# Performance work log

Measured on AMD Instinct MI355X. Metric: run time of the kernel, lower is better.

## Reference

```python
import jax, jax.numpy as jnp
import numpy as np


def setup_inputs() -> dict:
    key = jax.random.key(0)
    ks = jax.random.split(key, 12)
    L, B, T, E, H = 8, 256, 8, 1024, 1024
    w_scale = 1.0 / np.sqrt(E + H)  # keep gates out of saturation (mimics Linear init scale)
    inp = {
        "x": jax.random.normal(ks[0], (B, T, E), dtype=jnp.float32),
        "h0": jax.random.normal(ks[1], (L, B, H), dtype=jnp.float32),
        "c0": jax.random.normal(ks[2], (L, B, H), dtype=jnp.float32),
        "Wu": jax.random.normal(ks[3], (L, E + H, H), dtype=jnp.float32) * w_scale,
        "bu": jax.random.normal(ks[4], (L, H), dtype=jnp.float32) * w_scale,
        "Wf": jax.random.normal(ks[5], (L, E + H, H), dtype=jnp.float32) * w_scale,
        "bf": jax.random.normal(ks[6], (L, H), dtype=jnp.float32) * w_scale,
        "Wo": jax.random.normal(ks[7], (L, E + H, H), dtype=jnp.float32) * w_scale,
        "bo": jax.random.normal(ks[8], (L, H), dtype=jnp.float32) * w_scale,
        "Wc": jax.random.normal(ks[9], (L, E + H, H), dtype=jnp.float32) * w_scale,
        "bc": jax.random.normal(ks[10], (L, H), dtype=jnp.float32) * w_scale,
    }
    return inp


def reference(x, h0, c0, Wu, bu, Wf, bf, Wo, bo, Wc, bc):
    # x: [B,T,E]; h0,c0: [L,B,H]; W*: [L,E+H,H]; b*: [L,H]
    # Faithful to source: num_cells layers, time loop over first num_cells steps (T == L here).
    L = h0.shape[0]
    h = jnp.transpose(h0, (1, 0, 2))  # [B,L,H]
    c = jnp.transpose(c0, (1, 0, 2))

    def step(carry, xt):  # xt: [B,E]
        h, c = carry
        inp = xt
        hs, cs = [], []
        for l in range(L):
            zh = jnp.concatenate([inp, h[:, l]], axis=-1)  # [B, E+H]
            u = jax.nn.sigmoid(zh @ Wu[l] + bu[l])
            f = jax.nn.sigmoid(zh @ Wf[l] + bf[l])
            o = jax.nn.sigmoid(zh @ Wo[l] + bo[l])
            c_tilde = jnp.tanh(zh @ Wc[l] + bc[l])
            c_new = f * c[:, l] + u * c_tilde
            h_new = o * jnp.tanh(c_new)
            hs.append(h_new)
            cs.append(c_new)
            inp = h_new
        h = jnp.stack(hs, axis=1)
        c = jnp.stack(cs, axis=1)
        return (h, c), (h_new, c_new)  # emit top-layer h_t, c_t

    (_, _), (hs, cs) = jax.lax.scan(step, (h, c), jnp.transpose(x, (1, 0, 2)))
    hidden_states = jnp.transpose(hs, (1, 0, 2))  # [B,T,H]
    memory_states = jnp.transpose(cs, (1, 0, 2))
    h_t = hidden_states[:, -1:, :]  # [B,1,H], matches torch slice-shape
    c_t = memory_states[:, -1:, :]
    return hidden_states, memory_states, h_t, c_t
```

## Files before the change

### kernel.cpp

```cpp
#include <hip/hip_runtime.h>
#include <hip/hip_bf16.h>

#define B_ 256
#define T_ 8
#define E_ 1024
#define H_ 1024
#define L_ 8
#define KD 2048
#define ND 4096

#define BM 256
#define BN 128
#define BK 64
#define ABYTES 32768
#define BUFBYTES 49152
#define NT (KD / BK)

typedef __bf16 bf16x8 __attribute__((ext_vector_type(8)));
typedef float floatx4 __attribute__((ext_vector_type(4)));

__device__ __forceinline__ float sigm(float x) { return 1.f / (1.f + __expf(-x)); }
__device__ __forceinline__ float tanh_(float x) { return 1.f - 2.f / (__expf(2.f * x) + 1.f); }

__device__ __forceinline__ void async16(const void* g, void* l) {
    __builtin_amdgcn_global_load_lds(
        (const __attribute__((address_space(1))) void*)g,
        (__attribute__((address_space(3))) void*)l, 16, 0, 0);
}

__global__ __launch_bounds__(256) void prep_weights_g(
    const float* __restrict__ src, __hip_bfloat16* __restrict__ WTt, int g)
{
    __shared__ float sm[64][33];
    int bid = blockIdx.x;
    int jt = bid & 31;
    int kt = (bid >> 5) & 31;
    int l  = bid >> 10;
    int tid = threadIdx.x;
    int j4  = tid & 7;
    int kl0 = tid >> 3;
#pragma unroll
    for (int r = 0; r < 2; ++r) {
        int kl = kl0 + r * 32;
        float4 v = *(const float4*)&src[((size_t)(l * KD + kt * 64 + kl)) * 1024 + jt * 32 + j4 * 4];
        sm[kl][j4 * 4 + 0] = v.x;
        sm[kl][j4 * 4 + 1] = v.y;
        sm[kl][j4 * 4 + 2] = v.z;
        sm[kl][j4 * 4 + 3] = v.w;
    }
    __syncthreads();
    int jw = tid >> 3;
    int ch = tid & 7;
    int kc = ch * 8;
    bf16x8 v;
#pragma unroll
    for (int i = 0; i < 8; ++i)
        v[i] = (__bf16)sm[kc + i][jw];
    int n   = jt * 32 + jw;
    int nn  = n * 4 + g;
    int nb  = nn >> 7;
    int row = nn & 127;
    int cs  = ch ^ (row & 7);
    size_t off = ((((size_t)l * 32 + nb) * 32 + kt) * 128 + row) * 64 + (size_t)cs * 8;
    *(bf16x8*)&WTt[off] = v;
}

__global__ __launch_bounds__(256) void prep_misc(
    const float* __restrict__ x,  const float* __restrict__ h0,
    const float* __restrict__ c0,
    const float* __restrict__ bu, const float* __restrict__ bfv,
    const float* __restrict__ bo, const float* __restrict__ bc,
    __hip_bfloat16* __restrict__ xbf, __hip_bfloat16* __restrict__ hb0,
    float* __restrict__ cbuf, float* __restrict__ bcat)
{
    size_t i = (size_t)blockIdx.x * 256 + threadIdx.x;
    const size_t NX = (size_t)B_ * T_ * E_;
    const size_t NH = (size_t)L_ * B_ * H_;
    if (i < NX) {
        xbf[i] = __float2bfloat16(x[i]);
    } else if (i < NX + NH) {
        size_t j = i - NX; hb0[j] = __float2bfloat16(h0[j]);
    } else if (i < NX + 2 * NH) {
        size_t j = i - NX - NH; cbuf[j] = c0[j];
    } else if (i < NX + 2 * NH + (size_t)L_ * ND) {
        size_t j = i - NX - 2 * NH;
        int l = (int)(j >> 12); int n = (int)(j & 4095);
        int jj = n >> 2; int g = n & 3;
        const float* bs = (g == 0) ? bu : (g == 1) ? bfv : (g == 2) ? bo : bc;
        bcat[j] = bs[l * 1024 + jj];
    }
}

__global__ __launch_bounds__(512) void lstm_step(
    int d, int tmin,
    const __hip_bfloat16* __restrict__ xbf,
    const __hip_bfloat16* __restrict__ WTt,
    const float* __restrict__ bcat,
    __hip_bfloat16* __restrict__ hb0,
    __hip_bfloat16* __restrict__ hb1,
    float* __restrict__ cbuf,
    float* __restrict__ out)
{
    __shared__ __align__(16) char smraw[3][BUFBYTES];

    int cell = blockIdx.x >> 5;
    int nb   = blockIdx.x & 31;
    int t = tmin + cell;
    int l = d - t;

    const __hip_bfloat16* hread  = (t & 1) ? hb1 : hb0;
    __hip_bfloat16*       hwrite = (t & 1) ? hb0 : hb1;

    const __hip_bfloat16* A1; int sA1;
    if (l == 0) { A1 = xbf + (size_t)t * E_;               sA1 = T_ * E_; }
    else        { A1 = hwrite + (size_t)(l - 1) * B_ * H_; sA1 = H_; }
    const __hip_bfloat16* A2 = hread + (size_t)l * B_ * H_;
    const __hip_bfloat16* Bt = WTt + (((size_t)l * 32 + nb) * 32) * 128 * 64;

    int tid  = threadIdx.x;
    int lane = tid & 63;
    int wid  = tid >> 6;
    int wm = (wid & 3) * 64;
    int wn = (wid >> 2) * 64;
    int lr   = lane & 15;
    int quad = lane >> 4;

    int srow = tid >> 3;
    int c    = (tid & 7) ^ (srow & 7);
    const __hip_bfloat16* pA1[4];
    const __hip_bfloat16* pA2[4];
#pragma unroll
    for (int s = 0; s < 4; ++s) {
        int row = s * 64 + srow;
        pA1[s] = A1 + (size_t)row * sA1 + c * 8;
        pA2[s] = A2 + (size_t)row * H_ + c * 8 - E_;
    }
    const __hip_bfloat16* pB0 = Bt + (size_t)tid * 8;
    int ldsWaveOff = wid * 1024;

    auto stage = [&](int kt, int buf) {
        char* dst = smraw[buf];
        int k0 = kt * BK;
        bool first = (k0 < E_);
#pragma unroll
        for (int s = 0; s < 4; ++s) {
            const __hip_bfloat16* g = (first ? pA1[s] : pA2[s]) + k0;
            async16(g, dst + s * 8192 + ldsWaveOff);
        }
#pragma unroll
        for (int s = 0; s < 2; ++s) {
            async16(pB0 + (size_t)kt * 8192 + s * 4096, dst + ABYTES + s * 8192 + ldsWaveOff);
        }
    };

    floatx4 acc[4][4];
    floatx4 zero = {0.f, 0.f, 0.f, 0.f};
#pragma unroll
    for (int mi = 0; mi < 4; ++mi)
#pragma unroll
        for (int ni = 0; ni < 4; ++ni) acc[mi][ni] = zero;

    stage(0, 0);
    stage(1, 1);
    asm volatile("s_waitcnt vmcnt(6)" ::: "memory");
    __builtin_amdgcn_s_barrier();

    for (int kt = 0; kt < NT; ++kt) {
        const int cur = kt % 3;
        const __hip_bfloat16* sm  = (const __hip_bfloat16*)smraw[cur];
        const __hip_bfloat16* smB = sm + ABYTES / 2;

        {
            int xo = ((quad ^ (lr & 7)) * 8);
            bf16x8 af[4], bfr[4];
#pragma unroll
            for (int mi = 0; mi < 4; ++mi)
                af[mi] = *(const bf16x8*)&sm[(wm + mi * 16 + lr) * 64 + xo];
#pragma unroll
            for (int ni = 0; ni < 4; ++ni)
                bfr[ni] = *(const bf16x8*)&smB[(wn + ni * 16 + lr) * 64 + xo];
            if (kt + 2 < NT) stage(kt + 2, (kt + 2) % 3);
            __builtin_amdgcn_s_barrier();
            asm volatile("s_waitcnt lgkmcnt(0)" ::: "memory");
            __builtin_amdgcn_s_setprio(1);
#pragma unroll
            for (int mi = 0; mi < 4; ++mi)
#pragma unroll
                for (int ni = 0; ni < 4; ++ni)
                    acc[mi][ni] = __builtin_amdgcn_mfma_f32_16x16x32_bf16(
                        af[mi], bfr[ni], acc[mi][ni], 0, 0, 0);
            __builtin_amdgcn_s_setprio(0);
            __builtin_amdgcn_s_barrier();
        }

        {
            int xo = (((4 + quad) ^ (lr & 7)) * 8);
            bf16x8 af[4], bfr[4];
#pragma unroll
            for (int mi = 0; mi < 4; ++mi)
                af[mi] = *(const bf16x8*)&sm[(wm + mi * 16 + lr) * 64 + xo];
#pragma unroll
            for (int ni = 0; ni < 4; ++ni)
                bfr[ni] = *(const bf16x8*)&smB[(wn + ni * 16 + lr) * 64 + xo];
            __builtin_amdgcn_s_barrier();
            asm volatile("s_waitcnt lgkmcnt(0)" ::: "memory");
            __builtin_amdgcn_s_setprio(1);
#pragma unroll
            for (int mi = 0; mi < 4; ++mi)
#pragma unroll
                for (int ni = 0; ni < 4; ++ni)
                    acc[mi][ni] = __builtin_amdgcn_mfma_f32_16x16x32_bf16(
                        af[mi], bfr[ni], acc[mi][ni], 0, 0, 0);
            __builtin_amdgcn_s_setprio(0);
            if (kt < NT - 1) {
                if (kt + 2 < NT) { asm volatile("s_waitcnt vmcnt(6)" ::: "memory"); }
                else             { asm volatile("s_waitcnt vmcnt(0)" ::: "memory"); }
            }
            __builtin_amdgcn_s_barrier();
        }
    }

    float* outH  = out;
    float* outC  = out + (size_t)B_ * T_ * H_;
    float* outHt = out + 2 * (size_t)B_ * T_ * H_;
    float* outCt = outHt + (size_t)B_ * H_;
    auto sC = (float(*)[BN + 4])smraw[0];

    for (int q = 0; q < 4; ++q) {
        __syncthreads();
        if ((wid & 3) == q) {
#pragma unroll
            for (int mi = 0; mi < 4; ++mi)
#pragma unroll
                for (int ni = 0; ni < 4; ++ni)
#pragma unroll
                    for (int r = 0; r < 4; ++r)
                        sC[mi * 16 + quad * 4 + r][wn + ni * 16 + lr] = acc[mi][ni][r];
        }
        __syncthreads();
#pragma unroll
        for (int s = 0; s < 4; ++s) {
            int p = tid + s * 512;
            int r  = p >> 5;
            int jj = p & 31;
            float4 v  = *(float4*)&sC[r][jj * 4];
            float4 bb = *(const float4*)&bcat[(size_t)l * ND + nb * BN + jj * 4];
            float u  = sigm(v.x + bb.x);
            float f  = sigm(v.y + bb.y);
            float o  = sigm(v.z + bb.z);
            float ct = tanh_(v.w + bb.w);
            int b = q * 64 + r;
            int j = nb * 32 + jj;
            size_t ci = ((size_t)l * B_ + b) * H_ + j;
            float cn = f * cbuf[ci] + u * ct;
            cbuf[ci] = cn;
            float hn = o * tanh_(cn);
            hwrite[ci] = __float2bfloat16(hn);
            if (l == L_ - 1) {
                size_t oi = ((size_t)b * T_ + t) * H_ + j;
                outH[oi] = hn;
                outC[oi] = cn;
                if (t == T_ - 1) {
                    outHt[(size_t)b * H_ + j] = hn;
                    outCt[(size_t)b * H_ + j] = cn;
                }
            }
        }
    }
}

extern "C" void kernel_launch(void* const* d_in, const int* in_sizes, int n_in,
                              void* d_out, int out_size, void* d_ws, size_t ws_size,
                              hipStream_t stream)
{
    const float* x   = (const float*)d_in[0];
    const float* h0  = (const float*)d_in[1];
    const float* c0  = (const float*)d_in[2];
    const float* Wu  = (const float*)d_in[3];
    const float* bu  = (const float*)d_in[4];
    const float* Wf  = (const float*)d_in[5];
    const float* bfv = (const float*)d_in[6];
    const float* Wo  = (const float*)d_in[7];
    const float* bo  = (const float*)d_in[8];
    const float* Wc  = (const float*)d_in[9];
    const float* bc  = (const float*)d_in[10];
    float* out = (float*)d_out;

    char* ws = (char*)d_ws;
    __hip_bfloat16* WTt  = (__hip_bfloat16*)(ws);
    float*          bcat = (float*)(ws + 134217728);
    __hip_bfloat16* xbf  = (__hip_bfloat16*)(ws + 134348800);
    __hip_bfloat16* hb0  = (__hip_bfloat16*)(ws + 138543104);
    __hip_bfloat16* hb1  = (__hip_bfloat16*)(ws + 142737408);
    float*          cbuf = (float*)(ws + 146931712);

    hipLaunchKernelGGL(prep_weights_g, dim3(8192), dim3(256), 0, stream, Wu, WTt, 0);
    hipLaunchKernelGGL(prep_weights_g, dim3(8192), dim3(256), 0, stream, Wf, WTt, 1);
    hipLaunchKernelGGL(prep_weights_g, dim3(8192), dim3(256), 0, stream, Wo, WTt, 2);
    hipLaunchKernelGGL(prep_weights_g, dim3(8192), dim3(256), 0, stream, Wc, WTt, 3);
    size_t n2 = (size_t)2097152 * 3 + (size_t)L_ * ND;
    hipLaunchKernelGGL(prep_misc, dim3((unsigned)((n2 + 255) / 256)), dim3(256), 0, stream,
                       x, h0, c0, bu, bfv, bo, bc, xbf, hb0, cbuf, bcat);

    for (int dg = 0; dg <= (T_ - 1) + (L_ - 1); ++dg) {
        int tmin = dg > L_ - 1 ? dg - (L_ - 1) : 0;
        int tmax = dg < T_ - 1 ? dg : T_ - 1;
        int nc = tmax - tmin + 1;
        hipLaunchKernelGGL(lstm_step, dim3(nc * 32), dim3(512), 0, stream,
                           dg, tmin, xbf, WTt, bcat, hb0, hb1, cbuf, out);
    }
}
```

Baseline: 954.9 us.

## Split batch into two M-tiles with 256-thread blocks and double buffering

Halves the M tile from 256 to 128 rows so each wavefront diagonal launches twice as many blocks (64 per cell) with 256 threads each, raising CU occupancy on the small diagonals. The LDS pipeline drops from triple to double buffering, with the prefetch moved after both k-substeps behind a single barrier. Halving the tile also halves per-block reuse of the weight tiles, so weight traffic from L2/HBM doubles, and the pipeline now has less prefetch depth.

```diff
diff --git a/kernel.cpp b/kernel.cpp
--- a/kernel.cpp
+++ b/kernel.cpp
@@ -9,11 +9,11 @@
 #define KD 2048
 #define ND 4096
 
-#define BM 256
+#define BM 128
 #define BN 128
 #define BK 64
-#define ABYTES 32768
-#define BUFBYTES 49152
+#define ABYTES 16384
+#define BUFBYTES 32768
 #define NT (KD / BK)
 
 typedef __bf16 bf16x8 __attribute__((ext_vector_type(8)));
@@ -91,7 +91,7 @@
     }
 }
 
-__global__ __launch_bounds__(512) void lstm_step(
+__global__ __launch_bounds__(256) void lstm_step(
     int d, int tmin,
     const __hip_bfloat16* __restrict__ xbf,
     const __hip_bfloat16* __restrict__ WTt,
@@ -101,10 +101,11 @@
     float* __restrict__ cbuf,
     float* __restrict__ out)
 {
-    __shared__ __align__(16) char smraw[3][BUFBYTES];
-
-    int cell = blockIdx.x >> 5;
+    __shared__ __align__(16) char smraw[2][BUFBYTES];
+
     int nb   = blockIdx.x & 31;
+    int mb   = (blockIdx.x >> 5) & 1;
+    int cell = blockIdx.x >> 6;
     int t = tmin + cell;
     int l = d - t;
 
@@ -120,8 +121,8 @@
     int tid  = threadIdx.x;
     int lane = tid & 63;
     int wid  = tid >> 6;
-    int wm = (wid & 3) * 64;
-    int wn = (wid >> 2) * 64;
+    int wm = (wid & 1) * 64;
+    int wn = (wid >> 1) * 64;
     int lr   = lane & 15;
     int quad = lane >> 4;
 
@@ -131,12 +132,12 @@
     const __hip_bfloat16* pA2[4];
 #pragma unroll
     for (int s = 0; s < 4; ++s) {
-        int row = s * 64 + srow;
+        int row = mb * BM + s * 32 + srow;
         pA1[s] = A1 + (size_t)row * sA1 + c * 8;
         pA2[s] = A2 + (size_t)row * H_ + c * 8 - E_;
     }
     const __hip_bfloat16* pB0 = Bt + (size_t)tid * 8;
-    int ldsWaveOff = wid * 1024;
+    int ldsWaveOff = wid << 10;
 
     auto stage = [&](int kt, int buf) {
         char* dst = smraw[buf];
@@ -145,11 +146,12 @@
 #pragma unroll
         for (int s = 0; s < 4; ++s) {
             const __hip_bfloat16* g = (first ? pA1[s] : pA2[s]) + k0;
-            async16(g, dst + s * 8192 + ldsWaveOff);
-        }
-#pragma unroll
-        for (int s = 0; s < 2; ++s) {
-            async16(pB0 + (size_t)kt * 8192 + s * 4096, dst + ABYTES + s * 8192 + ldsWaveOff);
+            async16(g, dst + s * 4096 + ldsWaveOff);
+        }
+#pragma unroll
+        for (int s = 0; s < 4; ++s) {
+            async16(pB0 + (size_t)kt * 8192 + s * 2048,
+                    dst + ABYTES + s * 4096 + ldsWaveOff);
         }
     };
 
@@ -162,16 +164,16 @@
 
     stage(0, 0);
     stage(1, 1);
-    asm volatile("s_waitcnt vmcnt(6)" ::: "memory");
+    asm volatile("s_waitcnt vmcnt(8)" ::: "memory");
     __builtin_amdgcn_s_barrier();
 
     for (int kt = 0; kt < NT; ++kt) {
-        const int cur = kt % 3;
-        const __hip_bfloat16* sm  = (const __hip_bfloat16*)smraw[cur];
+        const __hip_bfloat16* sm  = (const __hip_bfloat16*)smraw[kt & 1];
         const __hip_bfloat16* smB = sm + ABYTES / 2;
 
-        {
-            int xo = ((quad ^ (lr & 7)) * 8);
+#pragma unroll
+        for (int ks = 0; ks < 2; ++ks) {
+            int xo = (((ks * 4 + quad) ^ (lr & 7)) * 8);
             bf16x8 af[4], bfr[4];
 #pragma unroll
             for (int mi = 0; mi < 4; ++mi)
@@ -179,9 +181,8 @@
 #pragma unroll
             for (int ni = 0; ni < 4; ++ni)
                 bfr[ni] = *(const bf16x8*)&smB[(wn + ni * 16 + lr) * 64 + xo];
-            if (kt + 2 < NT) stage(kt + 2, (kt + 2) % 3);
-            __builtin_amdgcn_s_barrier();
             asm volatile("s_waitcnt lgkmcnt(0)" ::: "memory");
+            __builtin_amdgcn_sched_barrier(0);
             __builtin_amdgcn_s_setprio(1);
 #pragma unroll
             for (int mi = 0; mi < 4; ++mi)
@@ -190,32 +191,13 @@
                     acc[mi][ni] = __builtin_amdgcn_mfma_f32_16x16x32_bf16(
                         af[mi], bfr[ni], acc[mi][ni], 0, 0, 0);
             __builtin_amdgcn_s_setprio(0);
-            __builtin_amdgcn_s_barrier();
-        }
-
-        {
-            int xo = (((4 + quad) ^ (lr & 7)) * 8);
-            bf16x8 af[4], bfr[4];
-#pragma unroll
-            for (int mi = 0; mi < 4; ++mi)
-                af[mi] = *(const bf16x8*)&sm[(wm + mi * 16 + lr) * 64 + xo];
-#pragma unroll
-            for (int ni = 0; ni < 4; ++ni)
-                bfr[ni] = *(const bf16x8*)&smB[(wn + ni * 16 + lr) * 64 + xo];
-            __builtin_amdgcn_s_barrier();
-            asm volatile("s_waitcnt lgkmcnt(0)" ::: "memory");
-            __builtin_amdgcn_s_setprio(1);
-#pragma unroll
-            for (int mi = 0; mi < 4; ++mi)
-#pragma unroll
-                for (int ni = 0; ni < 4; ++ni)
-                    acc[mi][ni] = __builtin_amdgcn_mfma_f32_16x16x32_bf16(
-                        af[mi], bfr[ni], acc[mi][ni], 0, 0, 0);
-            __builtin_amdgcn_s_setprio(0);
-            if (kt < NT - 1) {
-                if (kt + 2 < NT) { asm volatile("s_waitcnt vmcnt(6)" ::: "memory"); }
-                else             { asm volatile("s_waitcnt vmcnt(0)" ::: "memory"); }
-            }
+        }
+
+        __builtin_amdgcn_s_barrier();
+        if (kt + 2 < NT) stage(kt + 2, kt & 1);
+        if (kt < NT - 1) {
+            if (kt + 2 < NT) { asm volatile("s_waitcnt vmcnt(8)" ::: "memory"); }
+            else             { asm volatile("s_waitcnt vmcnt(0)" ::: "memory"); }
             __builtin_amdgcn_s_barrier();
         }
     }
@@ -226,9 +208,9 @@
     float* outCt = outHt + (size_t)B_ * H_;
     auto sC = (float(*)[BN + 4])smraw[0];
 
-    for (int q = 0; q < 4; ++q) {
+    for (int q = 0; q < 2; ++q) {
         __syncthreads();
-        if ((wid & 3) == q) {
+        if ((wid & 1) == q) {
 #pragma unroll
             for (int mi = 0; mi < 4; ++mi)
 #pragma unroll
@@ -239,8 +221,8 @@
         }
         __syncthreads();
 #pragma unroll
-        for (int s = 0; s < 4; ++s) {
-            int p = tid + s * 512;
+        for (int s = 0; s < 8; ++s) {
+            int p = tid + s * 256;
             int r  = p >> 5;
             int jj = p & 31;
             float4 v  = *(float4*)&sC[r][jj * 4];
@@ -249,7 +231,7 @@
             float f  = sigm(v.y + bb.y);
             float o  = sigm(v.z + bb.z);
             float ct = tanh_(v.w + bb.w);
-            int b = q * 64 + r;
+            int b = mb * BM + q * 64 + r;
             int j = nb * 32 + jj;
             size_t ci = ((size_t)l * B_ + b) * H_ + j;
             float cn = f * cbuf[ci] + u * ct;
@@ -306,7 +288,7 @@
         int tmin = dg > L_ - 1 ? dg - (L_ - 1) : 0;
         int tmax = dg < T_ - 1 ? dg : T_ - 1;
         int nc = tmax - tmin + 1;
-        hipLaunchKernelGGL(lstm_step, dim3(nc * 32), dim3(512), 0, stream,
+        hipLaunchKernelGGL(lstm_step, dim3(nc * 64), dim3(256), 0, stream,
                            dg, tmin, xbf, WTt, bcat, hb0, hb1, cbuf, out);
     }
 }
```

Result: faster. 844.2 us (-11.6%).
